# Optimization experiments

Hardware: AMD Instinct MI355X
Metric: run time of the kernel (lower is better)

The kernel has to match this reference:

```python
import jax, jax.numpy as jnp
import numpy as np

D = 512      # dgm / hidden width
L = 3        # n_dgm_layers
B = 131072   # collocation batch
SCALE = 0.02 # init scale to keep gates unsaturated


def setup_inputs() -> dict:
    key = jax.random.key(0)
    ks = jax.random.split(key, 12)
    X = jax.random.normal(ks[0], (B, 2), jnp.float32)
    t = jax.random.uniform(ks[1], (B, 1), jnp.float32)
    # input layer: Linear(3, D)
    W_in = jax.random.normal(ks[2], (3, D), jnp.float32) * SCALE
    b_in = jnp.zeros((D,), jnp.float32)
    # dense hidden: Linear(D, D)
    W_h1 = jax.random.normal(ks[3], (D, D), jnp.float32) * SCALE
    b_h1 = jnp.zeros((D,), jnp.float32)
    # projection to dgm dims: Linear(D, D)
    W_hd = jax.random.normal(ks[4], (D, D), jnp.float32) * SCALE
    b_hd = jnp.zeros((D,), jnp.float32)
    # DGM layers: 12 linears each, order [Uz,Wz,Bz, Ug,Wg,Bg, Ur,Wr,Br, Uh,Wh,Bh]
    dgm_W = jax.random.normal(ks[5], (L, 12, D, D), jnp.float32) * SCALE
    dgm_b = jnp.zeros((L, 12, D), jnp.float32)
    # output head: Linear(D, 1)
    W_out = jax.random.normal(ks[6], (D, 1), jnp.float32) * SCALE
    b_out = jnp.zeros((1,), jnp.float32)
    return {"X": X, "t": t, "W_in": W_in, "b_in": b_in, "W_h1": W_h1,
            "b_h1": b_h1, "W_hd": W_hd, "b_hd": b_hd, "dgm_W": dgm_W,
            "dgm_b": dgm_b, "W_out": W_out, "b_out": b_out}


def reference(X, t, W_in, b_in, W_h1, b_h1, W_hd, b_hd, dgm_W, dgm_b, W_out, b_out):
    inp = jnp.concatenate([X, t], axis=1)          # [B, 3]
    x = jnp.tanh(inp @ W_in + b_in)                # input layer + tanh
    x = jnp.tanh(x @ W_h1 + b_h1)                  # hidden Linear + tanh
    x = x @ W_hd + b_hd                            # hidden -> dgm projection (no act)
    S1 = x
    S = x
    for l in range(L):                             # small fixed layer loop
        W = dgm_W[l]
        b = dgm_b[l]
        lin = lambda i, v: v @ W[i] + b[i]
        Z = jax.nn.sigmoid(lin(0, x) + lin(1, S) + lin(2, S1))
        G = jax.nn.sigmoid(lin(3, x) + lin(4, S1) + lin(5, S))
        R = jax.nn.sigmoid(lin(6, x) + lin(7, S) + lin(8, S1))
        H = jnp.tanh(lin(9, x) + lin(10, S * R) + lin(11, S1))
        S = (1.0 - G) * H + Z * S
    return S @ W_out + b_out                       # [B, 1]
```

## Files before the change

### kernel.cpp

```cpp
#include <hip/hip_runtime.h>
#include <stdint.h>

namespace {

constexpr int B_ROWS = 131072;

typedef __attribute__((ext_vector_type(8))) short bf16x8;
typedef __attribute__((ext_vector_type(4))) float f32x4;

__device__ __forceinline__ unsigned short f2bf(float f) {
  unsigned u = __builtin_bit_cast(unsigned, f);
  u += 0x7fffu + ((u >> 16) & 1u);
  return (unsigned short)(u >> 16);
}
__device__ __forceinline__ float bf2f(unsigned short h) {
  unsigned u = ((unsigned)h) << 16;
  return __builtin_bit_cast(float, u);
}
__device__ __forceinline__ float sigm(float v) { return 1.0f / (1.0f + __expf(-v)); }


__global__ void pack_t_k(const float* __restrict__ W, unsigned short* __restrict__ Wt) {
  int idx = blockIdx.x * 256 + threadIdx.x;
  int n = idx >> 9, k = idx & 511;
  Wt[idx] = f2bf(W[(k << 9) + n]);
}

__global__ void pack_zgr_k(const float* __restrict__ dgmW, unsigned short* __restrict__ Wt) {
  long idx = (long)blockIdx.x * 256 + threadIdx.x;
  int l = (int)(idx / (1536 * 1024));
  int rest = (int)(idx - (long)l * (1536 * 1024));
  int n = rest >> 10, k = rest & 1023;
  int g = n >> 9, nn = n & 511;
  const int xi0[3] = {0, 3, 6};
  const int xi1[3] = {2, 4, 8};
  const int si[3] = {1, 5, 7};
  float v;
  if (k < 512)
    v = dgmW[(((long)(l * 12 + xi0[g]) << 9) + k) * 512 + nn] +
        dgmW[(((long)(l * 12 + xi1[g]) << 9) + k) * 512 + nn];
  else
    v = dgmW[(((long)(l * 12 + si[g]) << 9) + (k - 512)) * 512 + nn];
  Wt[idx] = f2bf(v);
}

__global__ void pack_h_k(const float* __restrict__ dgmW, unsigned short* __restrict__ Wt) {
  long idx = (long)blockIdx.x * 256 + threadIdx.x;
  int l = (int)(idx / (512 * 1024));
  int rest = (int)(idx - (long)l * (512 * 1024));
  int n = rest >> 10, k = rest & 1023;
  float v;
  if (k < 512)
    v = dgmW[(((long)(l * 12 + 9) << 9) + k) * 512 + n] +
        dgmW[(((long)(l * 12 + 11) << 9) + k) * 512 + n];
  else
    v = dgmW[(((long)(l * 12 + 10) << 9) + (k - 512)) * 512 + n];
  Wt[idx] = f2bf(v);
}

__global__ void pack_bias_k(const float* __restrict__ dgmb, float* __restrict__ bzgr,
                            float* __restrict__ bh) {
  int idx = blockIdx.x * 256 + threadIdx.x;
  if (idx >= 3 * 2048) return;
  int l = idx >> 11, n = idx & 2047;
  const float* bl = dgmb + l * 12 * 512;
  if (n < 1536) {
    int g = n >> 9, nn = n & 511;
    bzgr[l * 1536 + n] =
        bl[(g * 3 + 0) * 512 + nn] + bl[(g * 3 + 1) * 512 + nn] + bl[(g * 3 + 2) * 512 + nn];
  } else {
    int nn = n - 1536;
    bh[l * 512 + nn] = bl[9 * 512 + nn] + bl[10 * 512 + nn] + bl[11 * 512 + nn];
  }
}

__global__ void front0_k(const float* __restrict__ X, const float* __restrict__ t,
                         const float* __restrict__ Win, const float* __restrict__ bin,
                         unsigned short* __restrict__ x0, long row0) {
  long idx = (long)blockIdx.x * 256 + threadIdx.x;
  long r = idx >> 9;
  int c = (int)(idx & 511);
  long gr = row0 + r;
  float a = X[gr * 2] * Win[c] + X[gr * 2 + 1] * Win[512 + c] + t[gr] * Win[1024 + c] + bin[c];
  x0[idx] = f2bf(tanhf(a));
}

__global__ void head_k(const unsigned short* __restrict__ S, const float* __restrict__ Wout,
                       const float* __restrict__ bout, float* __restrict__ out, long row0) {
  const int lane = threadIdx.x & 63, wid = threadIdx.x >> 6;
  const long r = (long)blockIdx.x * 4 + wid;
  bf16x8 sv = *(const bf16x8*)&S[r * 512 + lane * 8];
  float sum = 0.f;
#pragma unroll
  for (int i = 0; i < 8; ++i) sum += bf2f((unsigned short)sv[i]) * Wout[lane * 8 + i];
#pragma unroll
  for (int off = 32; off > 0; off >>= 1) sum += __shfl_down(sum, off);
  if (lane == 0) out[row0 + r] = sum + bout[0];
}

template <int EPI, int KT, int LOGKT, int NCOL>
__global__ __launch_bounds__(512, 2) void gemmP_k(
    const unsigned short* __restrict__ a0, const unsigned short* __restrict__ a1,
    const unsigned short* __restrict__ wt, const float* __restrict__ bias,
    unsigned short* __restrict__ o0, unsigned short* __restrict__ o1,
    unsigned short* __restrict__ o2, const unsigned short* __restrict__ e0,
    const unsigned short* __restrict__ e1, int njobs, int jpb) {
  constexpr int K = KT * 64;
  extern __shared__ unsigned short lds[];
  const int tid = threadIdx.x;
  const int lane = tid & 63, wid = tid >> 6;
  const int wm = wid >> 2, wn = wid & 3;
  const int lr = lane & 15, kk = lane >> 4;

  const int G = gridDim.x;
  const int q = G >> 3, rr = G & 7;
  const int xcd = (int)blockIdx.x & 7, lo = (int)blockIdx.x >> 3;
  const int bsw = ((xcd < rr) ? xcd * (q + 1) : rr * (q + 1) + (xcd - rr) * q) + lo;
  const int j0 = bsw * jpb;
  if (j0 >= njobs) return;
  const int nj = min(jpb, njobs - j0);
  const int nseq = nj << LOGKT;

  const int gp8 = ((kk ^ ((lr >> 1) & 3)) << 3);
  const int a_rd = (wm * 128 + lr) * 32 + gp8;
  const int b_rd = 16384 + (wn * 64 + lr) * 32 + gp8;
  const int r0 = tid >> 2, gl0 = (tid & 3) ^ ((r0 >> 1) & 3);
  const int c1 = tid + 512, r1 = c1 >> 2, gl1 = (c1 & 3) ^ ((r1 >> 1) & 3);
  const int aL0 = r0 * 512 + gl0 * 8, aL1 = r1 * 512 + gl1 * 8;
  const size_t bL0 = (size_t)r0 * K + gl0 * 8, bL1 = (size_t)r1 * K + gl1 * 8;
  const int dL0 = tid * 8, dL1 = (tid + 512) * 8;

  f32x4 acc[8][4] = {};
  bf16x8 af[4], bf[4];

  auto stA = [&](int s2, int ks) {
    if (s2 >= nseq) return;
    const int jj = j0 + (s2 >> LOGKT);
    const int mt = jj / NCOL;
    const int kt2 = s2 & (KT - 1);
    const unsigned short* src = (KT == 16 && (kt2 & 8)) ? a1 : a0;
    const long pb = (long)mt * 131072 + (kt2 & 7) * 64 + ks * 32;
    const int d = ((s2 & 1) << 15) + ks * 8192;
    __builtin_amdgcn_global_load_lds(
        (const __attribute__((address_space(1))) void*)(src + pb + aL0),
        (__attribute__((address_space(3))) void*)(lds + d + dL0), 16, 0, 0);
    __builtin_amdgcn_global_load_lds(
        (const __attribute__((address_space(1))) void*)(src + pb + aL1),
        (__attribute__((address_space(3))) void*)(lds + d + dL1), 16, 0, 0);
  };
  auto stB = [&](int s2, int ks) {
    if (s2 >= nseq) return;
    const int jj = j0 + (s2 >> LOGKT);
    const int col = jj % NCOL;
    const int kt2 = s2 & (KT - 1);
    const size_t pb = (size_t)col * (256 * K) + kt2 * 64 + ks * 32;
    const int d = ((s2 & 1) << 15) + 16384 + ks * 8192;
    __builtin_amdgcn_global_load_lds(
        (const __attribute__((address_space(1))) void*)(wt + pb + bL0),
        (__attribute__((address_space(3))) void*)(lds + d + dL0), 16, 0, 0);
    __builtin_amdgcn_global_load_lds(
        (const __attribute__((address_space(1))) void*)(wt + pb + bL1),
        (__attribute__((address_space(3))) void*)(lds + d + dL1), 16, 0, 0);
  };
  auto ldA = [&](int cbo, int mh, int ks) {
#pragma unroll
    for (int m = 0; m < 4; ++m)
      af[m] = *(const bf16x8*)(lds + cbo + ks * 8192 + a_rd + mh * 2048 + m * 512);
  };
  auto ldB = [&](int cbo, int ks) {
#pragma unroll
    for (int n = 0; n < 4; ++n)
      bf[n] = *(const bf16x8*)(lds + cbo + ks * 8192 + b_rd + n * 512);
  };
  auto mmq = [&](int mh) {
    __builtin_amdgcn_s_setprio(1);
#pragma unroll
    for (int m = 0; m < 4; ++m)
#pragma unroll
      for (int n = 0; n < 4; ++n)
        acc[mh * 4 + m][n] =
            __builtin_amdgcn_mfma_f32_16x16x32_bf16(af[m], bf[n], acc[mh * 4 + m][n], 0, 0, 0);
    __builtin_amdgcn_s_setprio(0);
  };

  stB(0, 0);
  stA(0, 0);
  stB(0, 1);
  stA(0, 1);
  stB(1, 0);
  stA(1, 0);
  stB(1, 1);
  asm volatile("s_waitcnt vmcnt(5)" ::: "memory");
  __builtin_amdgcn_s_barrier();

  for (int s = 0; s < nseq; ++s) {
    const int cbo = (s & 1) << 15;
    const bool deep = (s + 4 <= nseq);
    ldB(cbo, 0);
    ldA(cbo, 0, 0);
    stA(s + 1, 1);
    __builtin_amdgcn_s_barrier();
    mmq(0);
    __builtin_amdgcn_s_barrier();
    ldA(cbo, 1, 0);
    stB(s + 2, 0);
    __builtin_amdgcn_s_barrier();
    mmq(1);
    if (deep)
      asm volatile("s_waitcnt vmcnt(5)" ::: "memory");
    else
      asm volatile("s_waitcnt vmcnt(0)" ::: "memory");
    __builtin_amdgcn_s_barrier();
    ldB(cbo, 1);
    ldA(cbo, 0, 1);
    stA(s + 2, 0);
    __builtin_amdgcn_s_barrier();
    mmq(0);
    __builtin_amdgcn_s_barrier();
    ldA(cbo, 1, 1);
    stB(s + 2, 1);
    __builtin_amdgcn_s_barrier();
    mmq(1);
    if (deep)
      asm volatile("s_waitcnt vmcnt(5)" ::: "memory");
    else
      asm volatile("s_waitcnt vmcnt(0)" ::: "memory");
    __builtin_amdgcn_s_barrier();

    if ((s & (KT - 1)) == (KT - 1)) {
      const int jj = j0 + (s >> LOGKT);
      const long brow = (long)(jj / NCOL) * 256;
      const int bcol = (jj % NCOL) * 256;
#pragma unroll
      for (int m = 0; m < 8; ++m) {
#pragma unroll
        for (int n = 0; n < 4; ++n) {
          const int col = bcol + wn * 64 + n * 16 + lr;
          const float bs = bias[col];
#pragma unroll
          for (int j = 0; j < 4; ++j) {
            const long row = brow + wm * 128 + m * 16 + kk * 4 + j;
            float v = acc[m][n][j] + bs;
            if constexpr (EPI == 0) {
              o0[row * 512 + col] = f2bf(tanhf(v));
            } else if constexpr (EPI == 1) {
              unsigned short b = f2bf(v);
              o0[row * 512 + col] = b;
              o1[row * 512 + col] = b;
            } else if constexpr (EPI == 2) {
              const int g = col >> 9;
              const int nn = col & 511;
              const float sgv = sigm(v);
              if (g == 0) {
                o0[row * 512 + nn] = f2bf(sgv * bf2f(e0[row * 512 + nn]));
              } else if (g == 1) {
                o1[row * 512 + nn] = f2bf(1.0f - sgv);
              } else {
                o2[row * 512 + nn] = f2bf(sgv * bf2f(e0[row * 512 + nn]));
              }
            } else {
              const float h = tanhf(v);
              const float omg = bf2f(e0[row * 512 + col]);
              const float zs = bf2f(e1[row * 512 + col]);
              o0[row * 512 + col] = f2bf(omg * h + zs);
            }
            acc[m][n][j] = 0.0f;
          }
        }
      }
    }
  }
}

}

extern "C" void kernel_launch(void* const* d_in, const int* in_sizes, int n_in,
                              void* d_out, int out_size, void* d_ws, size_t ws_size,
                              hipStream_t stream) {
  const float* X = (const float*)d_in[0];
  const float* t = (const float*)d_in[1];
  const float* W_in = (const float*)d_in[2];
  const float* b_in = (const float*)d_in[3];
  const float* W_h1 = (const float*)d_in[4];
  const float* b_h1 = (const float*)d_in[5];
  const float* W_hd = (const float*)d_in[6];
  const float* b_hd = (const float*)d_in[7];
  const float* dgm_W = (const float*)d_in[8];
  const float* dgm_b = (const float*)d_in[9];
  const float* W_out = (const float*)d_in[10];
  const float* b_out = (const float*)d_in[11];
  float* out = (float*)d_out;
  char* ws = (char*)d_ws;

  (void)hipFuncSetAttribute((const void*)&gemmP_k<0, 8, 3, 2>,
                            hipFuncAttributeMaxDynamicSharedMemorySize, 131072);
  (void)hipFuncSetAttribute((const void*)&gemmP_k<1, 8, 3, 2>,
                            hipFuncAttributeMaxDynamicSharedMemorySize, 131072);
  (void)hipFuncSetAttribute((const void*)&gemmP_k<2, 16, 4, 6>,
                            hipFuncAttributeMaxDynamicSharedMemorySize, 131072);
  (void)hipFuncSetAttribute((const void*)&gemmP_k<3, 16, 4, 2>,
                            hipFuncAttributeMaxDynamicSharedMemorySize, 131072);

  size_t off = 0;
  auto alloc = [&](size_t bytes) {
    size_t o = off;
    off = (off + bytes + 255) & ~(size_t)255;
    return o;
  };
  size_t o_wth1 = alloc((size_t)512 * 512 * 2);
  size_t o_wthd = alloc((size_t)512 * 512 * 2);
  size_t o_wtzgr = alloc((size_t)3 * 1536 * 1024 * 2);
  size_t o_wth = alloc((size_t)3 * 512 * 1024 * 2);
  size_t o_bzgr = alloc((size_t)3 * 1536 * 4);
  size_t o_bh = alloc((size_t)3 * 512 * 4);
  size_t actoff = off;

  unsigned short* wth1 = (unsigned short*)(ws + o_wth1);
  unsigned short* wthd = (unsigned short*)(ws + o_wthd);
  unsigned short* wtzgr = (unsigned short*)(ws + o_wtzgr);
  unsigned short* wth = (unsigned short*)(ws + o_wth);
  float* bzgr = (float*)(ws + o_bzgr);
  float* bh = (float*)(ws + o_bh);

  size_t avail = ws_size > actoff ? ws_size - actoff : 0;
  int nch = 1;
  while (nch < 256 && (size_t)(B_ROWS / nch) * 512 * 2 * 5 > avail) nch <<= 1;
  const int R = B_ROWS / nch;
  unsigned short* xb = (unsigned short*)(ws + actoff);
  unsigned short* Sb = xb + (size_t)R * 512;
  unsigned short* ZSb = Sb + (size_t)R * 512;
  unsigned short* OGb = ZSb + (size_t)R * 512;
  unsigned short* SRb = OGb + (size_t)R * 512;

  pack_t_k<<<1024, 256, 0, stream>>>(W_h1, wth1);
  pack_t_k<<<1024, 256, 0, stream>>>(W_hd, wthd);
  pack_zgr_k<<<18432, 256, 0, stream>>>(dgm_W, wtzgr);
  pack_h_k<<<6144, 256, 0, stream>>>(dgm_W, wth);
  pack_bias_k<<<24, 256, 0, stream>>>(dgm_b, bzgr, bh);

  const int MT = R / 256;
  auto cfg = [](int njobs, int& jpb, int& G) {
    jpb = (njobs + 255) / 256;
    G = (njobs + jpb - 1) / jpb;
  };
  int nj2 = 2 * MT, jpb2, G2;
  cfg(nj2, jpb2, G2);
  int nj6 = 6 * MT, jpb6, G6;
  cfg(nj6, jpb6, G6);

  for (int c = 0; c < nch; ++c) {
    long row0 = (long)c * R;
    front0_k<<<R * 2, 256, 0, stream>>>(X, t, W_in, b_in, ZSb, row0);
    gemmP_k<0, 8, 3, 2><<<G2, 512, 131072, stream>>>(ZSb, ZSb, wth1, b_h1, OGb, nullptr,
                                                     nullptr, nullptr, nullptr, nj2, jpb2);
    gemmP_k<1, 8, 3, 2><<<G2, 512, 131072, stream>>>(OGb, OGb, wthd, b_hd, xb, Sb, nullptr,
                                                     nullptr, nullptr, nj2, jpb2);
    for (int l = 0; l < 3; ++l) {
      gemmP_k<2, 16, 4, 6><<<G6, 512, 131072, stream>>>(
          xb, Sb, wtzgr + (size_t)l * 1536 * 1024, bzgr + l * 1536, ZSb, OGb, SRb, Sb,
          nullptr, nj6, jpb6);
      gemmP_k<3, 16, 4, 2><<<G2, 512, 131072, stream>>>(
          xb, SRb, wth + (size_t)l * 512 * 1024, bh + l * 512, Sb, nullptr, nullptr, OGb,
          ZSb, nj2, jpb2);
    }
    head_k<<<R / 4, 256, 0, stream>>>(Sb, W_out, b_out, out, row0);
  }
}
```

Measured before the change: 3.419 ms.

## Double-buffer MFMA fragment registers to overlap LDS reads with matrix math

```diff
diff --git a/kernel.cpp b/kernel.cpp
--- a/kernel.cpp
+++ b/kernel.cpp
@@ -131,7 +131,7 @@
   const int dL0 = tid * 8, dL1 = (tid + 512) * 8;
 
   f32x4 acc[8][4] = {};
-  bf16x8 af[4], bf[4];
+  bf16x8 afA[4], afB[4], bfA[4], bfB[4];
 
   auto stA = [&](int s2, int ks) {
     if (s2 >= nseq) return;
@@ -162,26 +162,24 @@
         (const __attribute__((address_space(1))) void*)(wt + pb + bL1),
         (__attribute__((address_space(3))) void*)(lds + d + dL1), 16, 0, 0);
   };
-  auto ldA = [&](int cbo, int mh, int ks) {
-#pragma unroll
-    for (int m = 0; m < 4; ++m)
-      af[m] = *(const bf16x8*)(lds + cbo + ks * 8192 + a_rd + mh * 2048 + m * 512);
-  };
-  auto ldB = [&](int cbo, int ks) {
-#pragma unroll
-    for (int n = 0; n < 4; ++n)
-      bf[n] = *(const bf16x8*)(lds + cbo + ks * 8192 + b_rd + n * 512);
-  };
-  auto mmq = [&](int mh) {
-    __builtin_amdgcn_s_setprio(1);
-#pragma unroll
-    for (int m = 0; m < 4; ++m)
-#pragma unroll
-      for (int n = 0; n < 4; ++n)
-        acc[mh * 4 + m][n] =
-            __builtin_amdgcn_mfma_f32_16x16x32_bf16(af[m], bf[n], acc[mh * 4 + m][n], 0, 0, 0);
-    __builtin_amdgcn_s_setprio(0);
-  };
+
+#define LDA(dst, cbo_, mh, ks_)                                                           \
+  _Pragma("unroll") for (int _m = 0; _m < 4; ++_m) dst[_m] =                              \
+      *(const bf16x8*)(lds + (cbo_) + (ks_)*8192 + a_rd + (mh)*2048 + _m * 512);
+
+#define LDB(dst, cbo_, ks_)                                                               \
+  _Pragma("unroll") for (int _n = 0; _n < 4; ++_n) dst[_n] =                              \
+      *(const bf16x8*)(lds + (cbo_) + (ks_)*8192 + b_rd + _n * 512);
+
+#define MMQ(mh, AF, BF)                                                                   \
+  do {                                                                                    \
+    __builtin_amdgcn_s_setprio(1);                                                        \
+    _Pragma("unroll") for (int _m = 0; _m < 4; ++_m) _Pragma("unroll") for (int _n = 0;   \
+                                                                            _n < 4; ++_n) \
+        acc[(mh)*4 + _m][_n] = __builtin_amdgcn_mfma_f32_16x16x32_bf16(                   \
+            AF[_m], BF[_n], acc[(mh)*4 + _m][_n], 0, 0, 0);                               \
+    __builtin_amdgcn_s_setprio(0);                                                        \
+  } while (0)
 
   stB(0, 0);
   stA(0, 0);
@@ -190,41 +188,44 @@
   stB(1, 0);
   stA(1, 0);
   stB(1, 1);
-  asm volatile("s_waitcnt vmcnt(5)" ::: "memory");
+  asm volatile("s_waitcnt vmcnt(10)" ::: "memory");
   __builtin_amdgcn_s_barrier();
+  LDB(bfA, 0, 0);
+  LDA(afA, 0, 0, 0);
 
   for (int s = 0; s < nseq; ++s) {
     const int cbo = (s & 1) << 15;
+    const int cbn = cbo ^ 32768;
     const bool deep = (s + 4 <= nseq);
-    ldB(cbo, 0);
-    ldA(cbo, 0, 0);
+    LDA(afB, cbo, 1, 0);
     stA(s + 1, 1);
     __builtin_amdgcn_s_barrier();
-    mmq(0);
-    __builtin_amdgcn_s_barrier();
-    ldA(cbo, 1, 0);
-    stB(s + 2, 0);
-    __builtin_amdgcn_s_barrier();
-    mmq(1);
+    MMQ(0, afA, bfA);
+    __builtin_amdgcn_s_barrier();
     if (deep)
-      asm volatile("s_waitcnt vmcnt(5)" ::: "memory");
+      asm volatile("s_waitcnt vmcnt(8)" ::: "memory");
     else
       asm volatile("s_waitcnt vmcnt(0)" ::: "memory");
-    __builtin_amdgcn_s_barrier();
-    ldB(cbo, 1);
-    ldA(cbo, 0, 1);
+    LDB(bfB, cbo, 1);
+    LDA(afA, cbo, 0, 1);
+    stB(s + 2, 0);
+    __builtin_amdgcn_s_barrier();
+    MMQ(1, afB, bfA);
+    __builtin_amdgcn_s_barrier();
+    LDA(afB, cbo, 1, 1);
     stA(s + 2, 0);
     __builtin_amdgcn_s_barrier();
-    mmq(0);
-    __builtin_amdgcn_s_barrier();
-    ldA(cbo, 1, 1);
-    stB(s + 2, 1);
-    __builtin_amdgcn_s_barrier();
-    mmq(1);
+    MMQ(0, afA, bfB);
+    __builtin_amdgcn_s_barrier();
     if (deep)
-      asm volatile("s_waitcnt vmcnt(5)" ::: "memory");
+      asm volatile("s_waitcnt vmcnt(8)" ::: "memory");
     else
       asm volatile("s_waitcnt vmcnt(0)" ::: "memory");
+    LDB(bfA, cbn, 0);
+    LDA(afA, cbn, 0, 0);
+    stB(s + 2, 1);
+    __builtin_amdgcn_s_barrier();
+    MMQ(1, afB, bfB);
     __builtin_amdgcn_s_barrier();
 
     if ((s & (KT - 1)) == (KT - 1)) {
@@ -270,6 +271,9 @@
       }
     }
   }
+#undef LDA
+#undef LDB
+#undef MMQ
 }
 
 }
```

Result: no change. 3.422 ms (+0.1%).
